# Kernel tuning notes

Measured on AMD Instinct MI355X. Metric: run time of the kernel, lower is better.

Reference implementation:

```python
import jax, jax.numpy as jnp
import numpy as np

B, T, LQ, LC = 8, 256, 20, 10
DIM, H = 128, 8
VDIM, WDIM, CDIM = 1024, 300, 50
WORDS, CHARS = 10000, 100


def _build_edges(T, B):
    """Replicates build_graph_edges(hops=2) + build_semantic_edges + build_query_edges,
    then expand_edge_index_for_batch with num_nodes = T + 1.  Static numpy (jit-safe)."""
    N = T + 1
    es = []
    for h in (1, 2):  # temporal edges, 2 hops (indices replicate original code exactly)
        i = np.arange(T - h)
        es += [np.stack([i, i + h]), np.stack([i + h, i])]
    i = np.arange(T)  # query<->segment edges inside build_graph_edges
    z = np.zeros(T, dtype=np.int64)
    es += [np.stack([z, i + 1]), np.stack([i + 1, z])]
    temporal = np.concatenate(es, axis=1)
    a, b = np.triu_indices(T, k=1)  # torch.combinations(arange(T), r=2)
    sem = np.concatenate([np.stack([a, b]), np.stack([b, a])], axis=1)
    qe = np.stack([np.concatenate([[0], np.arange(1, T + 1)]),
                   np.concatenate([np.arange(1, T + 1), [0]])])
    off = (np.arange(B, dtype=np.int64) * N)[None, :, None]
    expand = lambda e: (e[:, None, :].astype(np.int64) + off).reshape(2, -1)
    return np.concatenate([expand(temporal), expand(sem), expand(qe)], axis=1)


def setup_inputs() -> dict:
    key = jax.random.key(0)
    ks = jax.random.split(key, 16)
    w = lambda k, shape: jax.random.normal(k, shape, jnp.float32) * 0.02
    return {
        "word_ids": jax.random.randint(ks[0], (B, LQ), 0, WORDS),
        "char_ids": jax.random.randint(ks[1], (B, LQ, LC), 0, CHARS),
        "video_features": jax.random.normal(ks[2], (B, T, VDIM), jnp.float32),
        "v_mask": jnp.ones((B, T), jnp.float32),
        "q_mask": jnp.ones((B, LQ), jnp.float32),
        "word_emb": w(ks[3], (WORDS, WDIM)),
        "char_emb": w(ks[4], (CHARS, CDIM)),
        "W_embed": w(ks[5], (WDIM + CDIM, DIM)), "b_embed": jnp.zeros((DIM,), jnp.float32),
        "W_vproj": w(ks[6], (VDIM, DIM)), "b_vproj": jnp.zeros((DIM,), jnp.float32),
        "W_enc": w(ks[7], (DIM, DIM)), "b_enc": jnp.zeros((DIM,), jnp.float32),
        "Wq": w(ks[8], (DIM, DIM)), "bq": jnp.zeros((DIM,), jnp.float32),
        "Wk": w(ks[9], (DIM, DIM)), "bk": jnp.zeros((DIM,), jnp.float32),
        "Wv": w(ks[10], (DIM, DIM)), "bv": jnp.zeros((DIM,), jnp.float32),
        "Wskip": w(ks[11], (DIM, DIM)), "bskip": jnp.zeros((DIM,), jnp.float32),
        "W_start": w(ks[12], (DIM, 1)), "b_start": jnp.zeros((1,), jnp.float32),
        "W_end": w(ks[13], (DIM, 1)), "b_end": jnp.zeros((1,), jnp.float32),
    }


def reference(word_ids, char_ids, video_features, v_mask, q_mask,
              word_emb, char_emb, W_embed, b_embed, W_vproj, b_vproj,
              W_enc, b_enc, Wq, bq, Wk, bk, Wv, bv, Wskip, bskip,
              W_start, b_start, W_end, b_end):
    enc = lambda x, m: jax.nn.relu(x @ W_enc + b_enc) * m[..., None]  # shared feature encoder (stand-in)
    # video branch
    vfeat = enc(video_features @ W_vproj + b_vproj, v_mask)            # [B, T, DIM]
    # query branch: word + char embeddings -> dim, encode, mean-pool
    qemb = jnp.concatenate([word_emb[word_ids], char_emb[char_ids].mean(axis=2)], axis=-1)
    qfeat = enc(qemb @ W_embed + b_embed, q_mask).mean(axis=1)         # [B, DIM]
    nodes = jnp.concatenate([qfeat[:, None, :], vfeat], axis=1)        # [B, N, DIM], N = T+1
    Bn, N, _ = nodes.shape
    Nn = Bn * N
    xf = nodes.reshape(Nn, DIM)
    edges = jnp.asarray(_build_edges(N - 1, Bn))                       # [2, E] static
    src, dst = edges[0], edges[1]                                      # PyG: messages x_j=src -> target i=dst
    hd = DIM // H
    q = (xf @ Wq + bq).reshape(Nn, H, hd)
    k = (xf @ Wk + bk).reshape(Nn, H, hd)
    v = (xf @ Wv + bv).reshape(Nn, H, hd)
    # TransformerConv: per-edge attention logits, segment-softmax over incoming edges
    logits = (q[dst] * k[src]).sum(-1) / float(np.sqrt(hd))            # [E, H]
    mx = jax.ops.segment_max(logits, dst, num_segments=Nn)
    ex = jnp.exp(logits - mx[dst])
    den = jax.ops.segment_sum(ex, dst, num_segments=Nn)
    alpha = ex / (den[dst] + 1e-16)
    agg = jax.ops.segment_sum(alpha[:, :, None] * v[src], dst, num_segments=Nn)  # [Nn, H, hd]
    out = agg.reshape(Nn, DIM) + xf @ Wskip + bskip                    # root_weight skip connection
    out = out.reshape(Bn, N, DIM)
    start_logits = (out[:, 1:] @ W_start + b_start)[..., 0]            # [B, T]
    end_logits = (out[:, 1:] @ W_end + b_end)[..., 0]                  # [B, T]
    return start_logits, end_logits
```

## Files before the change

kernel.cpp:

```cpp
#include <hip/hip_runtime.h>
#include <hip/hip_bf16.h>
#include <math.h>

#define B_ 8
#define T_ 256
#define LQ_ 20
#define LC_ 10
#define DIM_ 128
#define N_ 257
#define NN_ (B_*N_)

__global__ __launch_bounds__(1024) void kNODE(
    const float* __restrict__ video, const float* __restrict__ Wv,
    const float* __restrict__ bvp,
    const float* __restrict__ We, const float* __restrict__ be,
    const float* __restrict__ vmask,
    const int* __restrict__ word_ids, const int* __restrict__ char_ids,
    const float* __restrict__ word_emb, const float* __restrict__ char_emb,
    const float* __restrict__ W_embed, const float* __restrict__ b_embed,
    const float* __restrict__ q_mask,
    const float* __restrict__ Wq, const float* __restrict__ bq,
    const float* __restrict__ Wk, const float* __restrict__ bk,
    const float* __restrict__ Wvv, const float* __restrict__ bval,
    const float* __restrict__ Ws, const float* __restrict__ bs,
    float* __restrict__ q, float* __restrict__ k,
    float* __restrict__ v, float* __restrict__ sk,
    float* __restrict__ eq)
{
  __shared__ float Vl[8][1028];
  __shared__ float4 ps8[8][8][32];
  __shared__ float hl[8][132];
  __shared__ float xe[8][132];
  const int blk = blockIdx.x, tid = threadIdx.x;
  const float* Wm[4] = {Wq, Wk, Wvv, Ws};
  const float* bm[4] = {bq, bk, bval, bs};
  float* om[4] = {q, k, v, sk};

  if (blk < 256) {
    const int r0 = blk * 8;
    {
      const float4* src = reinterpret_cast<const float4*>(video + (size_t)r0 * 1024);
      #pragma unroll
      for (int i = 0; i < 2; ++i) {
        const int idx4 = tid + i * 1024;
        const int r = idx4 >> 8, f = idx4 & 255;
        reinterpret_cast<float4*>(&Vl[r][0])[f] = src[r * 256 + f];
      }
    }
    __syncthreads();
    const int jc = tid & 31, rg = tid >> 5;
    {
      const int ke = rg >> 2, rp = rg & 3;
      const int ra = 2 * rp, rb = ra + 1;
      const float4* W4 = reinterpret_cast<const float4*>(Wv) + jc;
      const float* va = &Vl[ra][ke * 128];
      const float* vb = &Vl[rb][ke * 128];
      float4 a0 = {0,0,0,0}, a1 = {0,0,0,0};
      #pragma unroll 8
      for (int kk = 0; kk < 128; ++kk) {
        const float4 w = W4[(size_t)(ke * 128 + kk) * 32];
        const float x0 = va[kk], x1 = vb[kk];
        a0.x += x0*w.x; a0.y += x0*w.y; a0.z += x0*w.z; a0.w += x0*w.w;
        a1.x += x1*w.x; a1.y += x1*w.y; a1.z += x1*w.z; a1.w += x1*w.w;
      }
      ps8[ke][ra][jc] = a0;
      ps8[ke][rb][jc] = a1;
    }
    __syncthreads();
    if (tid < 256) {
      const int row = tid >> 5, c4 = tid & 31;
      float4 s = reinterpret_cast<const float4*>(bvp)[c4];
      #pragma unroll
      for (int ke = 0; ke < 8; ++ke) {
        const float4 p = ps8[ke][row][c4];
        s.x += p.x; s.y += p.y; s.z += p.z; s.w += p.w;
      }
      *reinterpret_cast<float4*>(&hl[row][4 * c4]) = s;
    }
    __syncthreads();
    {
      const int j = tid & 127, row = tid >> 7;
      float e = be[j];
      const float* hr = &hl[row][0];
      #pragma unroll 8
      for (int kk = 0; kk < 128; ++kk) e += hr[kk] * We[kk * 128 + j];
      e = fmaxf(e, 0.f) * vmask[r0 + row];
      xe[row][j] = e;
    }
    __syncthreads();
    {
      const int m = tid >> 8, row = (tid >> 5) & 7;
      const float4* W4p = reinterpret_cast<const float4*>(Wm[m]) + jc;
      float4 ac = reinterpret_cast<const float4*>(bm[m])[jc];
      const float* xr = &xe[row][0];
      #pragma unroll 8
      for (int kk = 0; kk < 128; ++kk) {
        const float4 w = W4p[kk * 32];
        const float x = xr[kk];
        ac.x += x*w.x; ac.y += x*w.y; ac.z += x*w.z; ac.w += x*w.w;
      }
      const int vr = r0 + row;
      const int node = (vr >> 8) * 257 + 1 + (vr & 255);
      *reinterpret_cast<float4*>(om[m] + (size_t)node * 128 + 4 * jc) = ac;
    }
  } else {
    const int qi = blk - 256;
    const int b = qi / 20, lq = qi - b * 20;
    float* emb = &Vl[0][0];
    float* ps  = emb + 352;
    float* hq  = emb + 608;
    float* pe  = emb + 736;
    const int wid = word_ids[b * LQ_ + lq];
    for (int m = tid; m < 300; m += 1024) emb[m] = word_emb[(size_t)wid * 300 + m];
    if (tid < 50) {
      float s = 0.f;
      #pragma unroll
      for (int l = 0; l < 10; ++l) {
        const int cid = char_ids[(b * LQ_ + lq) * 10 + l];
        s += char_emb[cid * 50 + tid];
      }
      emb[300 + tid] = s * 0.1f;
    }
    __syncthreads();
    const int j = tid & 127, half = tid >> 7;
    if (tid < 256) {
      float a = 0.f;
      const float* Wcol = W_embed + (size_t)(half * 175) * 128 + j;
      const float* eh = emb + half * 175;
      #pragma unroll 5
      for (int m = 0; m < 175; ++m) a += eh[m] * Wcol[(size_t)m * 128];
      ps[half * 128 + j] = a;
    }
    __syncthreads();
    if (tid < 128) hq[tid] = ps[tid] + ps[128 + tid] + b_embed[tid];
    __syncthreads();
    if (tid < 256) {
      float e = 0.f;
      #pragma unroll 8
      for (int kk = 0; kk < 64; ++kk)
        e += hq[half * 64 + kk] * We[(half * 64 + kk) * 128 + j];
      pe[half * 128 + j] = e;
    }
    __syncthreads();
    if (tid < 128) {
      float ev = pe[tid] + pe[128 + tid] + be[tid];
      ev = fmaxf(ev, 0.f) * q_mask[b * LQ_ + lq];
      eq[(size_t)qi * 128 + tid] = ev;
    }
  }
}

__device__ __forceinline__ float cntf(int dnode, int s) {
  if (dnode == 256) return (s == 0 ? 1.f : 0.f) + (s == 255 ? 1.f : 0.f);
  float c = (s != dnode) ? 1.f : 0.f;
  if (s == 0) c += 1.f;
  if (s == dnode - 1) c += 2.f;
  if (s == dnode + 1 && dnode <= 254) c += 1.f;
  if (s == dnode - 2 && dnode >= 2) c += 1.f;
  if (s == dnode + 2 && dnode <= 253) c += 1.f;
  return c;
}

__global__ __launch_bounds__(256) void kATTN(
    const float* __restrict__ q, const float* __restrict__ k,
    const float* __restrict__ v, const float* __restrict__ eq,
    const float* __restrict__ Wk, const float* __restrict__ bk,
    const float* __restrict__ Wvv, const float* __restrict__ bval,
    float* __restrict__ npart, float* __restrict__ dpart)
{
  __shared__ float Kl[16][128];
  __shared__ float Vl[16][128];
  __shared__ float m0[128];
  const int d0 = blockIdx.x * 32;
  const int y  = blockIdx.y;
  const int b  = blockIdx.z;
  const int tid = threadIdx.x;
  const int base = b * 257;
  const int s0 = y * 16;
  {
    const float4* ksrc = reinterpret_cast<const float4*>(k + (size_t)(base + s0) * 128);
    const float4* vsrc = reinterpret_cast<const float4*>(v + (size_t)(base + s0) * 128);
    float4* kd = reinterpret_cast<float4*>(Kl);
    float4* vd = reinterpret_cast<float4*>(Vl);
    #pragma unroll
    for (int i = 0; i < 2; ++i) {
      kd[tid + i * 256] = ksrc[tid + i * 256];
      vd[tid + i * 256] = vsrc[tid + i * 256];
    }
  }
  if (y == 0 && tid < 128) {
    float s = 0.f;
    #pragma unroll 4
    for (int lq = 0; lq < LQ_; ++lq) s += eq[((size_t)b * LQ_ + lq) * 128 + tid];
    m0[tid] = s * (1.f / LQ_);
  }
  const int dd = tid >> 3, h = tid & 7;
  const int dnode = d0 + dd + 1;
  const float* qrow = q + (size_t)(base + dnode) * 128 + h * 16;
  const float4 qq0 = *(const float4*)(qrow + 0);
  const float4 qq1 = *(const float4*)(qrow + 4);
  const float4 qq2 = *(const float4*)(qrow + 8);
  const float4 qq3 = *(const float4*)(qrow + 12);
  __syncthreads();
  if (y == 0) {
    const int j = tid & 127, half = tid >> 7;
    const float* W = half ? Wvv : Wk;
    float acc = half ? bval[j] : bk[j];
    #pragma unroll 8
    for (int kk = 0; kk < 128; ++kk) acc += m0[kk] * W[kk * 128 + j];
    if (half) Vl[0][j] = acc; else Kl[0][j] = acc;
  }
  __syncthreads();

  float den = 0.f;
  float4 o0 = {0,0,0,0}, o1 = {0,0,0,0}, o2 = {0,0,0,0}, o3 = {0,0,0,0};
  #pragma unroll 2
  for (int s = 0; s < 16; ++s) {
    const float* krow = &Kl[s][h * 16];
    const float4 k0 = *(const float4*)(krow + 0);
    const float4 k1 = *(const float4*)(krow + 4);
    const float4 k2 = *(const float4*)(krow + 8);
    const float4 k3 = *(const float4*)(krow + 12);
    float dt = qq0.x*k0.x + qq0.y*k0.y + qq0.z*k0.z + qq0.w*k0.w
             + qq1.x*k1.x + qq1.y*k1.y + qq1.z*k1.z + qq1.w*k1.w
             + qq2.x*k2.x + qq2.y*k2.y + qq2.z*k2.z + qq2.w*k2.w
             + qq3.x*k3.x + qq3.y*k3.y + qq3.z*k3.z + qq3.w*k3.w;
    const float c = cntf(dnode, s0 + s);
    const float pw = c * __expf(dt * 0.25f);
    den += pw;
    const float* vrow = &Vl[s][h * 16];
    const float4 v0 = *(const float4*)(vrow + 0);
    const float4 v1 = *(const float4*)(vrow + 4);
    const float4 v2 = *(const float4*)(vrow + 8);
    const float4 v3 = *(const float4*)(vrow + 12);
    o0.x += pw*v0.x; o0.y += pw*v0.y; o0.z += pw*v0.z; o0.w += pw*v0.w;
    o1.x += pw*v1.x; o1.y += pw*v1.y; o1.z += pw*v1.z; o1.w += pw*v1.w;
    o2.x += pw*v2.x; o2.y += pw*v2.y; o2.z += pw*v2.z; o2.w += pw*v2.w;
    o3.x += pw*v3.x; o3.y += pw*v3.y; o3.z += pw*v3.z; o3.w += pw*v3.w;
  }
  const size_t pb = ((size_t)y * 8 + b) * 256 + d0;
  float* np = npart + (pb + dd) * 128 + h * 16;
  *reinterpret_cast<float4*>(np + 0)  = o0;
  *reinterpret_cast<float4*>(np + 4)  = o1;
  *reinterpret_cast<float4*>(np + 8)  = o2;
  *reinterpret_cast<float4*>(np + 12) = o3;
  dpart[(pb + dd) * 8 + h] = den;
}

__global__ __launch_bounds__(256) void kRED(
    const float* __restrict__ npart, const float* __restrict__ dpart,
    const float* __restrict__ sk,
    const float* __restrict__ W_start, const float* __restrict__ b_start,
    const float* __restrict__ W_end, const float* __restrict__ b_end,
    float* __restrict__ out)
{
  __shared__ float red[16][2][2];
  const int d0 = blockIdx.x * 16;
  const int b = blockIdx.y;
  const int tid = threadIdx.x;
  const int base = b * 257;
  const int jB = tid & 127, shB = tid >> 7;
  const int hB = jB >> 4;
  const float wst = W_start[jB], wen = W_end[jB];
  #pragma unroll
  for (int dd8 = 0; dd8 < 8; ++dd8) {
    const int dd = shB * 8 + dd8;
    const int dst = d0 + dd;
    float num = 0.f, den = 0.f;
    #pragma unroll
    for (int y = 0; y < 16; ++y) {
      const size_t pb = ((size_t)y * 8 + b) * 256 + dst;
      num += npart[pb * 128 + jB];
      den += dpart[pb * 8 + hB];
    }
    const float o = num / (den + 1e-16f) + sk[(size_t)(base + dst + 1) * 128 + jB];
    float psum = o * wst, pesum = o * wen;
    #pragma unroll
    for (int off = 1; off < 64; off <<= 1) {
      psum += __shfl_xor(psum, off);
      pesum += __shfl_xor(pesum, off);
    }
    if ((tid & 63) == 0) { red[dd][jB >> 6][0] = psum; red[dd][jB >> 6][1] = pesum; }
  }
  __syncthreads();
  if (tid < 16) {
    out[b * 256 + d0 + tid]        = red[tid][0][0] + red[tid][1][0] + b_start[0];
    out[2048 + b * 256 + d0 + tid] = red[tid][0][1] + red[tid][1][1] + b_end[0];
  }
}

extern "C" void kernel_launch(void* const* d_in, const int* in_sizes, int n_in,
                              void* d_out, int out_size, void* d_ws, size_t ws_size,
                              hipStream_t stream) {
  const int*   word_ids = (const int*)d_in[0];
  const int*   char_ids = (const int*)d_in[1];
  const float* video    = (const float*)d_in[2];
  const float* v_mask   = (const float*)d_in[3];
  const float* q_mask   = (const float*)d_in[4];
  const float* word_emb = (const float*)d_in[5];
  const float* char_emb = (const float*)d_in[6];
  const float* W_embed  = (const float*)d_in[7];
  const float* b_embed  = (const float*)d_in[8];
  const float* W_vproj  = (const float*)d_in[9];
  const float* b_vproj  = (const float*)d_in[10];
  const float* W_enc    = (const float*)d_in[11];
  const float* b_enc    = (const float*)d_in[12];
  const float* Wq       = (const float*)d_in[13];
  const float* bq       = (const float*)d_in[14];
  const float* Wk       = (const float*)d_in[15];
  const float* bk       = (const float*)d_in[16];
  const float* Wv       = (const float*)d_in[17];
  const float* bv       = (const float*)d_in[18];
  const float* Wskip    = (const float*)d_in[19];
  const float* bskip    = (const float*)d_in[20];
  const float* W_start  = (const float*)d_in[21];
  const float* b_start  = (const float*)d_in[22];
  const float* W_end    = (const float*)d_in[23];
  const float* b_end    = (const float*)d_in[24];

  float* q     = (float*)d_ws;
  float* k     = q  + NN_ * DIM_;
  float* v     = k  + NN_ * DIM_;
  float* sk    = v  + NN_ * DIM_;
  float* eq    = sk + NN_ * DIM_;
  float* npart = eq + 160 * 128;
  float* dpart = npart + (size_t)16 * 8 * 256 * 128;

  hipLaunchKernelGGL(kNODE, dim3(416), dim3(1024), 0, stream,
    video, W_vproj, b_vproj, W_enc, b_enc, v_mask,
    word_ids, char_ids, word_emb, char_emb, W_embed, b_embed, q_mask,
    Wq, bq, Wk, bk, Wv, bv, Wskip, bskip, q, k, v, sk, eq);
  hipLaunchKernelGGL(kATTN, dim3(8, 16, 8), dim3(256), 0, stream,
    q, k, v, eq, Wk, bk, Wv, bv, npart, dpart);
  hipLaunchKernelGGL(kRED, dim3(16, 8), dim3(256), 0, stream,
    npart, dpart, sk, W_start, b_start, W_end, b_end, (float*)d_out);
}
```

Measured before the change: 72.80 us.

## Remap node-projection thread layout and halve attention source-chunk count

The video projection in kNODE is remapped so each 64-lane group covers 8 rows by 8 column-float4s, with a 4-way K split of 256 instead of an 8-way split of 128. The encoder GEMM moves to the same K-split-plus-reduction layout, adding one shared-memory reduction pass and barrier. Separately, kATTN now processes 32 source nodes per block instead of 16, which halves the grid along y and the number of partial numerator/denominator slabs that kRED must read and sum. This trades less partial-sum traffic and fewer blocks for more serial work per thread and less parallelism in attention.

```diff
diff --git a/kernel.cpp b/kernel.cpp
--- a/kernel.cpp
+++ b/kernel.cpp
@@ -28,7 +28,7 @@
     float* __restrict__ eq)
 {
   __shared__ float Vl[8][1028];
-  __shared__ float4 ps8[8][8][32];
+  __shared__ float4 ps4[4][8][33];
   __shared__ float hl[8][132];
   __shared__ float xe[8][132];
   const int blk = blockIdx.x, tid = threadIdx.x;
@@ -48,60 +48,78 @@
       }
     }
     __syncthreads();
-    const int jc = tid & 31, rg = tid >> 5;
+    const int g = tid >> 6, lane = tid & 63;
+    const int r = lane >> 3, c = lane & 7;
     {
-      const int ke = rg >> 2, rp = rg & 3;
-      const int ra = 2 * rp, rb = ra + 1;
-      const float4* W4 = reinterpret_cast<const float4*>(Wv) + jc;
-      const float* va = &Vl[ra][ke * 128];
-      const float* vb = &Vl[rb][ke * 128];
-      float4 a0 = {0,0,0,0}, a1 = {0,0,0,0};
+      const int ke = g >> 2, cg = g & 3;
+      const int col4 = cg * 8 + c;
+      const float4* W4 = reinterpret_cast<const float4*>(Wv) + col4;
+      const float* vr = &Vl[r][ke * 256];
+      float4 a = {0,0,0,0};
       #pragma unroll 8
-      for (int kk = 0; kk < 128; ++kk) {
-        const float4 w = W4[(size_t)(ke * 128 + kk) * 32];
-        const float x0 = va[kk], x1 = vb[kk];
-        a0.x += x0*w.x; a0.y += x0*w.y; a0.z += x0*w.z; a0.w += x0*w.w;
-        a1.x += x1*w.x; a1.y += x1*w.y; a1.z += x1*w.z; a1.w += x1*w.w;
-      }
-      ps8[ke][ra][jc] = a0;
-      ps8[ke][rb][jc] = a1;
+      for (int kk = 0; kk < 256; ++kk) {
+        const float4 w = W4[(size_t)(ke * 256 + kk) * 32];
+        const float x = vr[kk];
+        a.x += x*w.x; a.y += x*w.y; a.z += x*w.z; a.w += x*w.w;
+      }
+      ps4[ke][r][col4] = a;
     }
     __syncthreads();
     if (tid < 256) {
       const int row = tid >> 5, c4 = tid & 31;
       float4 s = reinterpret_cast<const float4*>(bvp)[c4];
       #pragma unroll
-      for (int ke = 0; ke < 8; ++ke) {
-        const float4 p = ps8[ke][row][c4];
+      for (int ke = 0; ke < 4; ++ke) {
+        const float4 p = ps4[ke][row][c4];
         s.x += p.x; s.y += p.y; s.z += p.z; s.w += p.w;
       }
       *reinterpret_cast<float4*>(&hl[row][4 * c4]) = s;
     }
     __syncthreads();
     {
-      const int j = tid & 127, row = tid >> 7;
-      float e = be[j];
-      const float* hr = &hl[row][0];
+      const int ke = g >> 2, cg = g & 3;
+      const int col4 = cg * 8 + c;
+      const float4* We4 = reinterpret_cast<const float4*>(We) + col4;
+      const float* hr = &hl[r][ke * 32];
+      float4 a = {0,0,0,0};
       #pragma unroll 8
-      for (int kk = 0; kk < 128; ++kk) e += hr[kk] * We[kk * 128 + j];
-      e = fmaxf(e, 0.f) * vmask[r0 + row];
-      xe[row][j] = e;
+      for (int kk = 0; kk < 32; ++kk) {
+        const float4 w = We4[(size_t)(ke * 32 + kk) * 32];
+        const float x = hr[kk];
+        a.x += x*w.x; a.y += x*w.y; a.z += x*w.z; a.w += x*w.w;
+      }
+      ps4[ke][r][col4] = a;
+    }
+    __syncthreads();
+    if (tid < 256) {
+      const int row = tid >> 5, c4 = tid & 31;
+      float4 s = reinterpret_cast<const float4*>(be)[c4];
+      #pragma unroll
+      for (int ke = 0; ke < 4; ++ke) {
+        const float4 p = ps4[ke][row][c4];
+        s.x += p.x; s.y += p.y; s.z += p.z; s.w += p.w;
+      }
+      const float mk = vmask[r0 + row];
+      s.x = fmaxf(s.x, 0.f) * mk; s.y = fmaxf(s.y, 0.f) * mk;
+      s.z = fmaxf(s.z, 0.f) * mk; s.w = fmaxf(s.w, 0.f) * mk;
+      *reinterpret_cast<float4*>(&xe[row][4 * c4]) = s;
     }
     __syncthreads();
     {
-      const int m = tid >> 8, row = (tid >> 5) & 7;
-      const float4* W4p = reinterpret_cast<const float4*>(Wm[m]) + jc;
-      float4 ac = reinterpret_cast<const float4*>(bm[m])[jc];
-      const float* xr = &xe[row][0];
+      const int m = g >> 2, cg = g & 3;
+      const int col4 = cg * 8 + c;
+      const float4* W4p = reinterpret_cast<const float4*>(Wm[m]) + col4;
+      float4 ac = reinterpret_cast<const float4*>(bm[m])[col4];
+      const float* xr = &xe[r][0];
       #pragma unroll 8
       for (int kk = 0; kk < 128; ++kk) {
-        const float4 w = W4p[kk * 32];
+        const float4 w = W4p[(size_t)kk * 32];
         const float x = xr[kk];
         ac.x += x*w.x; ac.y += x*w.y; ac.z += x*w.z; ac.w += x*w.w;
       }
-      const int vr = r0 + row;
-      const int node = (vr >> 8) * 257 + 1 + (vr & 255);
-      *reinterpret_cast<float4*>(om[m] + (size_t)node * 128 + 4 * jc) = ac;
+      const int vr2 = r0 + r;
+      const int node = (vr2 >> 8) * 257 + 1 + (vr2 & 255);
+      *reinterpret_cast<float4*>(om[m] + (size_t)node * 128 + 4 * col4) = ac;
     }
   } else {
     const int qi = blk - 256;
@@ -168,22 +186,22 @@
     const float* __restrict__ Wvv, const float* __restrict__ bval,
     float* __restrict__ npart, float* __restrict__ dpart)
 {
-  __shared__ float Kl[16][128];
-  __shared__ float Vl[16][128];
+  __shared__ float Kl[32][128];
+  __shared__ float Vl[32][128];
   __shared__ float m0[128];
   const int d0 = blockIdx.x * 32;
   const int y  = blockIdx.y;
   const int b  = blockIdx.z;
   const int tid = threadIdx.x;
   const int base = b * 257;
-  const int s0 = y * 16;
+  const int s0 = y * 32;
   {
     const float4* ksrc = reinterpret_cast<const float4*>(k + (size_t)(base + s0) * 128);
     const float4* vsrc = reinterpret_cast<const float4*>(v + (size_t)(base + s0) * 128);
     float4* kd = reinterpret_cast<float4*>(Kl);
     float4* vd = reinterpret_cast<float4*>(Vl);
     #pragma unroll
-    for (int i = 0; i < 2; ++i) {
+    for (int i = 0; i < 4; ++i) {
       kd[tid + i * 256] = ksrc[tid + i * 256];
       vd[tid + i * 256] = vsrc[tid + i * 256];
     }
@@ -215,7 +233,7 @@
   float den = 0.f;
   float4 o0 = {0,0,0,0}, o1 = {0,0,0,0}, o2 = {0,0,0,0}, o3 = {0,0,0,0};
   #pragma unroll 2
-  for (int s = 0; s < 16; ++s) {
+  for (int s = 0; s < 32; ++s) {
     const float* krow = &Kl[s][h * 16];
     const float4 k0 = *(const float4*)(krow + 0);
     const float4 k1 = *(const float4*)(krow + 4);
@@ -268,7 +286,7 @@
     const int dst = d0 + dd;
     float num = 0.f, den = 0.f;
     #pragma unroll
-    for (int y = 0; y < 16; ++y) {
+    for (int y = 0; y < 8; ++y) {
       const size_t pb = ((size_t)y * 8 + b) * 256 + dst;
       num += npart[pb * 128 + jB];
       den += dpart[pb * 8 + hB];
@@ -324,13 +342,13 @@
   float* sk    = v  + NN_ * DIM_;
   float* eq    = sk + NN_ * DIM_;
   float* npart = eq + 160 * 128;
-  float* dpart = npart + (size_t)16 * 8 * 256 * 128;
+  float* dpart = npart + (size_t)8 * 8 * 256 * 128;
 
   hipLaunchKernelGGL(kNODE, dim3(416), dim3(1024), 0, stream,
     video, W_vproj, b_vproj, W_enc, b_enc, v_mask,
     word_ids, char_ids, word_emb, char_emb, W_embed, b_embed, q_mask,
     Wq, bq, Wk, bk, Wv, bv, Wskip, bskip, q, k, v, sk, eq);
-  hipLaunchKernelGGL(kATTN, dim3(8, 16, 8), dim3(256), 0, stream,
+  hipLaunchKernelGGL(kATTN, dim3(8, 8, 8), dim3(256), 0, stream,
     q, k, v, eq, Wk, bk, Wv, bv, npart, dpart);
   hipLaunchKernelGGL(kRED, dim3(16, 8), dim3(256), 0, stream,
     npart, dpart, sk, W_start, b_start, W_end, b_end, (float*)d_out);
```

New measurement: 83.72 us. 1.15x slower.
